# Kernel optimization log

Measured on AMD Instinct MI355X. Metric: run time of the kernel, lower is better.

Reference implementation:

```python
import jax, jax.numpy as jnp
import numpy as np

B = 65536      # batch
C = 1000       # num_classes
D = 256        # feat_dim


def _l2norm(x, eps=1e-12):
    # matches F.normalize(dim=1): v / max(||v||_2, eps)
    n = jnp.linalg.norm(x, axis=1, keepdims=True)
    return x / jnp.maximum(n, eps)


def setup_inputs() -> dict:
    key = jax.random.key(0)
    k1, k2, k3, k4, k5 = jax.random.split(key, 5)
    bound = 1.0 / np.sqrt(D)
    X = jax.random.normal(k1, (B, D), dtype=jnp.float32)
    labels = jax.random.randint(k2, (B,), 0, C)
    signatures = jax.random.uniform(k3, (C, D), dtype=jnp.float32, minval=-bound, maxval=bound)
    b_means = jax.random.uniform(k4, (1, D), dtype=jnp.float32, minval=-bound, maxval=bound)
    b_covs = jax.random.normal(k5, (D, D), dtype=jnp.float32)
    return {"X": X, "labels": labels, "signatures": signatures,
            "b_means": b_means, "b_covs": b_covs}


def reference(X, labels, signatures, b_means, b_covs):
    # SVD-based whitening of background covariance (tiny DxD)
    cov = b_covs @ b_covs.T
    U, eig, _ = jnp.linalg.svd(cov)
    DU = (eig ** -0.5)[:, None] * U.T              # diag(eig^-1/2) @ U^T, [D, D]
    xHat = _l2norm((X - b_means) @ DU.T)           # [B, D]
    sHat = _l2norm(signatures @ DU.T)              # [C, D]
    ACE_targets = xHat @ sHat.T                    # [B, C] cosine scores
    labels = labels.astype(jnp.int32)
    numerator = jnp.take_along_axis(ACE_targets, labels[:, None], axis=1)[:, 0]
    # denominator = exp(true) + sum(exp(others)) == sum over all classes
    loss = -jnp.mean(numerator - jax.nn.logsumexp(ACE_targets, axis=1))
    return (loss, ACE_targets)
```

## Files before the change

kernel.cpp:

```cpp
#include <hip/hip_runtime.h>
#include <hip/hip_bf16.h>
#include <math.h>

#define D_ 256
#define B_ 65536
#define C_ 1000

typedef _Float16 f16x8 __attribute__((ext_vector_type(8)));
typedef float f32x4 __attribute__((ext_vector_type(4)));

__global__ __launch_bounds__(256) void cov_kernel(const float* __restrict__ bc,
                                                  double* __restrict__ C64,
                                                  double* __restrict__ acc) {
  __shared__ float Ash[32][260];
  __shared__ float Bsh2[32][260];
  const int b = blockIdx.x, bi = b >> 3, bj = b & 7;
  const int e = threadIdx.x;
  if (b == 0 && e == 0) *acc = 0.0;
#pragma unroll
  for (int s = 0; s < 32; ++s) {
    int lin = s * 256 + e;
    int rr = lin >> 8, cc = lin & 255;
    Ash[rr][cc] = bc[(bi * 32 + rr) * 256 + cc];
    Bsh2[rr][cc] = bc[(bj * 32 + rr) * 256 + cc];
  }
  __syncthreads();
  const int tx = e & 15, ty = e >> 4;
  double a00 = 0, a01 = 0, a10 = 0, a11 = 0;
#pragma unroll 8
  for (int k = 0; k < 256; ++k) {
    double ar0 = (double)Ash[ty][k], ar1 = (double)Ash[ty + 16][k];
    double br0 = (double)Bsh2[tx][k], br1 = (double)Bsh2[tx + 16][k];
    a00 += ar0 * br0; a01 += ar0 * br1;
    a10 += ar1 * br0; a11 += ar1 * br1;
  }
  const int r0 = bi * 32, c0 = bj * 32;
  C64[(size_t)(r0 + ty) * D_ + c0 + tx] = a00;
  C64[(size_t)(r0 + ty) * D_ + c0 + tx + 16] = a01;
  C64[(size_t)(r0 + ty + 16) * D_ + c0 + tx] = a10;
  C64[(size_t)(r0 + ty + 16) * D_ + c0 + tx + 16] = a11;
}

__global__ __launch_bounds__(256, 1) void chol_panel(double* __restrict__ A, int p) {
  const int j0 = p * 64;
  const int r = threadIdx.x;
  __shared__ double raw[2][64];
  double pr[64];
  const bool act = (r >= j0);
  const bool inpanel = act && (r < j0 + 64);
  if (act) {
#pragma unroll
    for (int k = 0; k < 64; ++k) pr[k] = A[(size_t)r * D_ + j0 + k];
  }
  if (inpanel) raw[0][r - j0] = pr[0];
  __syncthreads();
#pragma unroll
  for (int j = 0; j < 64; ++j) {
    const int col = j0 + j;
    const double d2 = raw[j & 1][j];
    double rs = (double)rsqrtf((float)d2);
    rs = rs * (1.5 - 0.5 * d2 * rs * rs);
    rs = rs * (1.5 - 0.5 * d2 * rs * rs);
    if (r >= col) {
      const double lr_ = pr[j] * rs;
      pr[j] = lr_;
#pragma unroll
      for (int k = j + 1; k < 64; ++k) pr[k] -= lr_ * (raw[j & 1][k] * rs);
    }
    if (j < 63) {
      if (r > col && r < j0 + 64) raw[(j + 1) & 1][r - j0] = pr[j + 1];
    }
    __syncthreads();
  }
  if (act) {
    const int kmax = (r - j0 < 63) ? (r - j0) : 63;
#pragma unroll
    for (int k = 0; k < 64; ++k)
      if (k <= kmax) A[(size_t)r * D_ + j0 + k] = pr[k];
  }
}

__global__ __launch_bounds__(256) void chol_trail(double* __restrict__ A, int p) {
  const int j0 = p * 64;
  const int t0 = j0 + 64;
  int b = blockIdx.x, I = 0;
  while (b >= I + 1) { b -= I + 1; ++I; }
  const int J = b;
  const int r0 = t0 + I * 64, c0 = t0 + J * 64;
  __shared__ double LR[64][67];
  __shared__ double LC[64][67];
  const int tid = threadIdx.x;
  for (int e = tid; e < 64 * 64; e += 256) {
    int rr = e >> 6, cc = e & 63;
    LR[rr][cc] = A[(size_t)(r0 + rr) * D_ + j0 + cc];
    LC[rr][cc] = A[(size_t)(c0 + rr) * D_ + j0 + cc];
  }
  __syncthreads();
  const int tx = tid & 15, ty = tid >> 4;
  double acc[4][4];
#pragma unroll
  for (int i = 0; i < 4; ++i)
#pragma unroll
    for (int j = 0; j < 4; ++j) acc[i][j] = 0.0;
#pragma unroll 4
  for (int k = 0; k < 64; ++k) {
    double a_[4], b_[4];
#pragma unroll
    for (int i = 0; i < 4; ++i) a_[i] = LR[ty + 16 * i][k];
#pragma unroll
    for (int j = 0; j < 4; ++j) b_[j] = LC[tx + 16 * j][k];
#pragma unroll
    for (int i = 0; i < 4; ++i)
#pragma unroll
      for (int j = 0; j < 4; ++j) acc[i][j] += a_[i] * b_[j];
  }
#pragma unroll
  for (int i = 0; i < 4; ++i) {
    const int grow = r0 + ty + 16 * i;
#pragma unroll
    for (int j = 0; j < 4; ++j) {
      const int gcol = c0 + tx + 16 * j;
      A[(size_t)grow * D_ + gcol] -= acc[i][j];
    }
  }
}

__global__ __launch_bounds__(256) void inv_kernel(const double* __restrict__ L,
                                                  _Float16* __restrict__ WbP,
                                                  _Float16* __restrict__ WbT) {
  const int c = blockIdx.x;
  const int tid = threadIdx.x;
  __shared__ double w[D_];
  __shared__ double rdi[D_];
  __shared__ double rhs[32];
  __shared__ double Ldd[32][33];
  w[tid] = 0.0;
  rdi[tid] = 1.0 / L[(size_t)tid * D_ + tid];
  __syncthreads();
  const int q0 = c >> 5;
  for (int q = q0; q < 8; ++q) {
    const int i0 = q * 32;
    const int ii = tid >> 3, s = tid & 7;
    const int i = i0 + ii;
    double part = 0.0;
    for (int k = c + s; k < i0; k += 8) part += L[(size_t)i * D_ + k] * w[k];
    part += __shfl_xor(part, 1, 64);
    part += __shfl_xor(part, 2, 64);
    part += __shfl_xor(part, 4, 64);
    if (s == 0) rhs[ii] = ((i == c) ? 1.0 : 0.0) - part;
    for (int e = tid; e < 32 * 32; e += 256) {
      int rr = e >> 5, cc = e & 31;
      Ldd[rr][cc] = L[(size_t)(i0 + rr) * D_ + i0 + cc];
    }
    __syncthreads();
    if (tid < 32) {
      double x = rhs[tid];
      double v = 0.0;
      for (int j = 0; j < 32; ++j) {
        double xj = __shfl(x, j, 64);
        double wj = xj * rdi[i0 + j];
        if (tid == j) v = wj;
        if (tid > j) x -= Ldd[tid][j] * wj;
      }
      w[i0 + tid] = v;
    }
    __syncthreads();
  }
  _Float16 h = (_Float16)(float)w[tid];
  WbT[(size_t)c * D_ + tid] = h;
  {
    const int g = tid >> 4, lrr = tid & 15;
    const int ks = c >> 5, lqq = (c >> 3) & 3, jj = c & 7;
    WbP[(size_t)(g * 8 + ks) * 512 + (size_t)(lqq * 16 + lrr) * 8 + jj] = h;
  }
}

__global__ void sig_kernel(const float* __restrict__ S, const _Float16* __restrict__ WbT,
                           _Float16* __restrict__ sHatP) {
  int c = blockIdx.x, i = threadIdx.x;
  const int g = c >> 4, lr = c & 15;
  const int ks = i >> 5, lq = (i >> 3) & 3, jj = i & 7;
  const size_t off = (size_t)(g * 8 + ks) * 512 + (size_t)(lq * 16 + lr) * 8 + jj;
  if (c >= C_) { sHatP[off] = (_Float16)0.0f; return; }
  __shared__ float srow[D_];
  __shared__ float wred[4];
  srow[i] = S[c * D_ + i];
  __syncthreads();
  float t = 0.f;
  for (int k = 0; k < D_; ++k) t += (float)WbT[k * D_ + i] * srow[k];
  float ss = t * t;
#pragma unroll
  for (int d = 1; d < 64; d <<= 1) ss += __shfl_xor(ss, d, 64);
  if ((i & 63) == 0) wred[i >> 6] = ss;
  __syncthreads();
  float tot = wred[0] + wred[1] + wred[2] + wred[3];
  float rn = 1.0f / fmaxf(sqrtf(tot), 1e-12f);
  sHatP[off] = (_Float16)(t * rn);
}

__global__ __launch_bounds__(512) void xform_kernel(const float* __restrict__ X,
                                                    const float* __restrict__ means,
                                                    const _Float16* __restrict__ WbP,
                                                    _Float16* __restrict__ xHat,
                                                    float* __restrict__ rnX) {
  __shared__ __align__(16) _Float16 Wsh[65536];
  __shared__ float msh[D_];
  const int tid = threadIdx.x;
  const int wid = tid >> 6, l = tid & 63, lr = l & 15, lq = l >> 4;
  const int rowbase = blockIdx.x * 128;
  const int arow = rowbase + wid * 16 + lr;
  if (tid < 256) msh[tid] = means[tid];
#pragma unroll
  for (int s = 0; s < 16; ++s) {
    const int off = (wid * 16 + s) * 512;
    __builtin_amdgcn_global_load_lds(
        (const __attribute__((address_space(1))) unsigned int*)(WbP + off + l * 8),
        (__attribute__((address_space(3))) unsigned int*)(&Wsh[off]), 16, 0, 0);
  }
  __syncthreads();

  f16x8 af[8];
#pragma unroll
  for (int ks = 0; ks < 8; ++ks) {
    const float* xp = X + (size_t)arow * D_ + lq * 8 + ks * 32;
    const float4 x0 = *(const float4*)(xp);
    const float4 x1 = *(const float4*)(xp + 4);
    const int mb = lq * 8 + ks * 32;
    af[ks][0] = (_Float16)(x0.x - msh[mb + 0]);
    af[ks][1] = (_Float16)(x0.y - msh[mb + 1]);
    af[ks][2] = (_Float16)(x0.z - msh[mb + 2]);
    af[ks][3] = (_Float16)(x0.w - msh[mb + 3]);
    af[ks][4] = (_Float16)(x1.x - msh[mb + 4]);
    af[ks][5] = (_Float16)(x1.y - msh[mb + 5]);
    af[ks][6] = (_Float16)(x1.z - msh[mb + 6]);
    af[ks][7] = (_Float16)(x1.w - msh[mb + 7]);
  }

  float ss[4] = {0.f, 0.f, 0.f, 0.f};
  const _Float16* bb = &Wsh[(size_t)l * 8];
  for (int ch = 0; ch < 2; ++ch) {
    f32x4 acc[8];
#pragma unroll
    for (int t = 0; t < 8; ++t) acc[t] = (f32x4){0.f, 0.f, 0.f, 0.f};
#pragma unroll
    for (int ks = 0; ks < 8; ++ks) {
#pragma unroll
      for (int t = 0; t < 8; ++t) {
        f16x8 bf = *(const f16x8*)(bb + (ch * 64 + t * 8 + ks) * 512);
        acc[t] = __builtin_amdgcn_mfma_f32_16x16x32_f16(af[ks], bf, acc[t], 0, 0, 0);
      }
    }
#pragma unroll
    for (int t = 0; t < 8; ++t) {
      const int col = ch * 128 + t * 16 + lr;
#pragma unroll
      for (int j = 0; j < 4; ++j) {
        const int row = rowbase + wid * 16 + lq * 4 + j;
        float v = acc[t][j];
        ss[j] += v * v;
        xHat[(size_t)row * D_ + col] = (_Float16)v;
      }
    }
  }
#pragma unroll
  for (int d = 1; d < 16; d <<= 1) {
#pragma unroll
    for (int j = 0; j < 4; ++j) ss[j] += __shfl_xor(ss[j], d, 64);
  }
  if (lr == 0) {
#pragma unroll
    for (int j = 0; j < 4; ++j) {
      const int row = rowbase + wid * 16 + lq * 4 + j;
      rnX[row] = 1.0f / fmaxf(sqrtf(ss[j]), 1e-12f);
    }
  }
}

__global__ __launch_bounds__(1024) void ace_kernel(const _Float16* __restrict__ xHat,
                                                   const _Float16* __restrict__ sHatP,
                                                   const float* __restrict__ rnX,
                                                   const int* __restrict__ labels,
                                                   float* __restrict__ outACE,
                                                   double* __restrict__ acc_loss) {
  __shared__ __align__(16) _Float16 Bsh[2][64 * 512];
  __shared__ float part[64];
  const int tid = threadIdx.x;
  const int wid = tid >> 6, l = tid & 63, lr = l & 15, lq = l >> 4;
  const int rowbase = blockIdx.x * 256;
  const int wrow = rowbase + wid * 16;

  f16x8 a[8];
  {
    const _Float16* ap = xHat + (size_t)(wrow + lr) * D_ + lq * 8;
#pragma unroll
    for (int ks = 0; ks < 8; ++ks) a[ks] = *(const f16x8*)(ap + ks * 32);
  }

  int lab[4]; float rx[4], ssum[4], num[4];
#pragma unroll
  for (int j = 0; j < 4; ++j) {
    int row = wrow + lq * 4 + j;
    lab[j] = labels[row];
    rx[j] = rnX[row];
    ssum[j] = 0.f; num[j] = 0.f;
  }

#define STAGE(bufi, chi) do {                                                        \
    const _Float16* _src = sHatP + (size_t)(chi) * 32768;                            \
    _Float16* _dst = &Bsh[bufi][0];                                                  \
    _Pragma("unroll")                                                                \
    for (int _s = 0; _s < 4; ++_s) {                                                 \
      const int _off = wid * 2048 + _s * 512;                                        \
      __builtin_amdgcn_global_load_lds(                                              \
          (const __attribute__((address_space(1))) unsigned int*)(_src + _off + l * 8), \
          (__attribute__((address_space(3))) unsigned int*)(_dst + _off), 16, 0, 0); \
    } } while (0)

  float* const outrow = outACE + (size_t)(wrow + lq * 4) * C_;

  STAGE(0, 0);
  __syncthreads();
  int buf = 0;
  for (int ch = 0; ch < 8; ++ch) {
    if (ch < 7) {
      STAGE(buf ^ 1, ch + 1);
      __builtin_amdgcn_sched_barrier(0);
    }
    const _Float16* bb = &Bsh[buf][(size_t)l * 8];
    f32x4 acc[8];
#pragma unroll
    for (int t = 0; t < 8; ++t) acc[t] = (f32x4){0.f, 0.f, 0.f, 0.f};
#pragma unroll
    for (int ks = 0; ks < 8; ++ks) {
#pragma unroll
      for (int t = 0; t < 8; ++t) {
        f16x8 bf = *(const f16x8*)(bb + (t * 8 + ks) * 512);
        acc[t] = __builtin_amdgcn_mfma_f32_16x16x32_f16(a[ks], bf, acc[t], 0, 0, 0);
      }
    }
#pragma unroll
    for (int t = 0; t < 8; ++t) {
      const int col = ch * 128 + t * 16 + lr;
      const bool valid = (col < C_);
#pragma unroll
      for (int j = 0; j < 4; ++j) {
        float v = acc[t][j] * rx[j];
        if (valid) outrow[(size_t)j * C_ + col] = v;
        ssum[j] += __expf(v - 1.0f);
        num[j] = (col == lab[j]) ? v : num[j];
      }
    }
    if (ch < 7) {
      __builtin_amdgcn_sched_barrier(0);
      asm volatile("s_waitcnt vmcnt(32)" ::: "memory");
      __builtin_amdgcn_s_barrier();
      __builtin_amdgcn_sched_barrier(0);
    }
    buf ^= 1;
  }
#undef STAGE

#pragma unroll
  for (int d2 = 1; d2 < 16; d2 <<= 1) {
#pragma unroll
    for (int j = 0; j < 4; ++j) {
      ssum[j] += __shfl_xor(ssum[j], d2, 64);
      num[j]  += __shfl_xor(num[j], d2, 64);
    }
  }
  if (lr == 0) {
    const float padcorr = 24.0f * __expf(-1.0f);
    float contrib = 0.f;
#pragma unroll
    for (int j = 0; j < 4; ++j)
      contrib += num[j] - (1.0f + __logf(ssum[j] - padcorr));
    part[wid * 4 + lq] = contrib;
  }
  __syncthreads();
  if (tid == 0) {
    float s = 0.f;
#pragma unroll
    for (int p2 = 0; p2 < 64; ++p2) s += part[p2];
    atomicAdd(acc_loss, (double)s);
  }
}

__global__ void fin_kernel(const double* a, float* out) {
  out[0] = (float)(-(*a) / (double)B_);
}

extern "C" void kernel_launch(void* const* d_in, const int* in_sizes, int n_in,
                              void* d_out, int out_size, void* d_ws, size_t ws_size,
                              hipStream_t stream) {
  const float* X      = (const float*)d_in[0];
  const int*   labels = (const int*)d_in[1];
  const float* S      = (const float*)d_in[2];
  const float* means  = (const float*)d_in[3];
  const float* bc     = (const float*)d_in[4];
  float* out = (float*)d_out;

  char* w = (char*)d_ws;
  double*    acc   = (double*)(w + 0);
  double*    C64   = (double*)(w + 256);
  _Float16*  WbP   = (_Float16*)(w + 524544);
  _Float16*  WbT   = (_Float16*)(w + 655616);
  _Float16*  sHatP = (_Float16*)(w + 786688);
  float*     rnX   = (float*)(w + 1310976);
  _Float16*  xHat  = (_Float16*)(w + 1573120);

  cov_kernel<<<64, 256, 0, stream>>>(bc, C64, acc);
  for (int p = 0; p < 4; ++p) {
    chol_panel<<<1, 256, 0, stream>>>(C64, p);
    int nt = 3 - p;
    if (nt > 0) chol_trail<<<nt * (nt + 1) / 2, 256, 0, stream>>>(C64, p);
  }
  inv_kernel<<<256, 256, 0, stream>>>(C64, WbP, WbT);
  sig_kernel<<<1024, 256, 0, stream>>>(S, WbT, sHatP);
  xform_kernel<<<512, 512, 0, stream>>>(X, means, WbP, xHat, rnX);
  ace_kernel<<<256, 1024, 0, stream>>>(xHat, sHatP, rnX, labels, out + 1, acc);
  fin_kernel<<<1, 1, 0, stream>>>(acc, out);
}
```

Before: 367.5 us.

## Fuse whitening transform into ACE kernel and finalize loss via last-block counter

Merges the X whitening/normalization GEMM into the ACE score kernel. The whitened rows are computed in registers, passed through swizzled LDS into the A-fragment layout, and never written to global memory as xHat/rnX. The separate finalize launch is replaced by an atomic counter, so the last block writes the mean loss. This removes a 32MB fp16 round trip and two kernel launches. In exchange each block holds 16 accumulator tiles, which raises register pressure, and the whole 128KB LDS is reused across phases with extra barriers.

Result: faster. 358.5 us (-2.5%).

```diff
diff --git a/kernel.cpp b/kernel.cpp
--- a/kernel.cpp
+++ b/kernel.cpp
@@ -11,12 +11,13 @@
 
 __global__ __launch_bounds__(256) void cov_kernel(const float* __restrict__ bc,
                                                   double* __restrict__ C64,
-                                                  double* __restrict__ acc) {
+                                                  double* __restrict__ acc,
+                                                  unsigned int* __restrict__ counter) {
   __shared__ float Ash[32][260];
   __shared__ float Bsh2[32][260];
   const int b = blockIdx.x, bi = b >> 3, bj = b & 7;
   const int e = threadIdx.x;
-  if (b == 0 && e == 0) *acc = 0.0;
+  if (b == 0 && e == 0) { *acc = 0.0; *counter = 0u; }
 #pragma unroll
   for (int s = 0; s < 32; ++s) {
     int lin = s * 256 + e;
@@ -198,24 +199,35 @@
   sHatP[off] = (_Float16)(t * rn);
 }
 
-__global__ __launch_bounds__(512) void xform_kernel(const float* __restrict__ X,
-                                                    const float* __restrict__ means,
-                                                    const _Float16* __restrict__ WbP,
-                                                    _Float16* __restrict__ xHat,
-                                                    float* __restrict__ rnX) {
-  __shared__ __align__(16) _Float16 Wsh[65536];
+__global__ __launch_bounds__(1024) void ace_kernel(const float* __restrict__ X,
+                                                   const float* __restrict__ means,
+                                                   const _Float16* __restrict__ WbP,
+                                                   const _Float16* __restrict__ sHatP,
+                                                   const int* __restrict__ labels,
+                                                   float* __restrict__ out,
+                                                   double* __restrict__ acc_loss,
+                                                   unsigned int* __restrict__ counter) {
+  __shared__ __align__(16) char ldsraw[131072];
   __shared__ float msh[D_];
+  __shared__ float part[64];
+  _Float16* const Wsh = (_Float16*)ldsraw;
+  char* const xsC = ldsraw;
+  _Float16* const Bsh = (_Float16*)ldsraw;
+  float* const outACE = out + 1;
+
   const int tid = threadIdx.x;
   const int wid = tid >> 6, l = tid & 63, lr = l & 15, lq = l >> 4;
-  const int rowbase = blockIdx.x * 128;
-  const int arow = rowbase + wid * 16 + lr;
+  const int rowbase = blockIdx.x * 256;
+  const int wrow = rowbase + wid * 16;
+  const int arow = wrow + lr;
+
   if (tid < 256) msh[tid] = means[tid];
 #pragma unroll
-  for (int s = 0; s < 16; ++s) {
-    const int off = (wid * 16 + s) * 512;
+  for (int s = 0; s < 8; ++s) {
+    const int off = (wid * 8 + s) * 512;
     __builtin_amdgcn_global_load_lds(
         (const __attribute__((address_space(1))) unsigned int*)(WbP + off + l * 8),
-        (__attribute__((address_space(3))) unsigned int*)(&Wsh[off]), 16, 0, 0);
+        (__attribute__((address_space(3))) unsigned int*)(Wsh + off), 16, 0, 0);
   }
   __syncthreads();
 
@@ -235,79 +247,67 @@
     af[ks][6] = (_Float16)(x1.z - msh[mb + 6]);
     af[ks][7] = (_Float16)(x1.w - msh[mb + 7]);
   }
-
+  f32x4 wacc[16];
+#pragma unroll
+  for (int u = 0; u < 16; ++u) wacc[u] = (f32x4){0.f, 0.f, 0.f, 0.f};
+  {
+    const _Float16* wb = Wsh + (size_t)l * 8;
+#pragma unroll
+    for (int ks = 0; ks < 8; ++ks) {
+#pragma unroll
+      for (int u = 0; u < 16; ++u) {
+        f16x8 bf = *(const f16x8*)(wb + (u * 8 + ks) * 512);
+        wacc[u] = __builtin_amdgcn_mfma_f32_16x16x32_f16(af[ks], bf, wacc[u], 0, 0, 0);
+      }
+    }
+  }
   float ss[4] = {0.f, 0.f, 0.f, 0.f};
-  const _Float16* bb = &Wsh[(size_t)l * 8];
-  for (int ch = 0; ch < 2; ++ch) {
-    f32x4 acc[8];
-#pragma unroll
-    for (int t = 0; t < 8; ++t) acc[t] = (f32x4){0.f, 0.f, 0.f, 0.f};
-#pragma unroll
-    for (int ks = 0; ks < 8; ++ks) {
-#pragma unroll
-      for (int t = 0; t < 8; ++t) {
-        f16x8 bf = *(const f16x8*)(bb + (ch * 64 + t * 8 + ks) * 512);
-        acc[t] = __builtin_amdgcn_mfma_f32_16x16x32_f16(af[ks], bf, acc[t], 0, 0, 0);
-      }
-    }
-#pragma unroll
-    for (int t = 0; t < 8; ++t) {
-      const int col = ch * 128 + t * 16 + lr;
-#pragma unroll
-      for (int j = 0; j < 4; ++j) {
-        const int row = rowbase + wid * 16 + lq * 4 + j;
-        float v = acc[t][j];
-        ss[j] += v * v;
-        xHat[(size_t)row * D_ + col] = (_Float16)v;
-      }
-    }
-  }
+#pragma unroll
+  for (int u = 0; u < 16; ++u)
+#pragma unroll
+    for (int j = 0; j < 4; ++j) ss[j] += wacc[u][j] * wacc[u][j];
 #pragma unroll
   for (int d = 1; d < 16; d <<= 1) {
 #pragma unroll
     for (int j = 0; j < 4; ++j) ss[j] += __shfl_xor(ss[j], d, 64);
   }
-  if (lr == 0) {
+  float rx[4];
+#pragma unroll
+  for (int j = 0; j < 4; ++j) rx[j] = 1.0f / fmaxf(sqrtf(ss[j]), 1e-12f);
+
+  __syncthreads();
+
+#pragma unroll
+  for (int u = 0; u < 16; ++u) {
 #pragma unroll
     for (int j = 0; j < 4; ++j) {
-      const int row = rowbase + wid * 16 + lq * 4 + j;
-      rnX[row] = 1.0f / fmaxf(sqrtf(ss[j]), 1e-12f);
-    }
-  }
-}
-
-__global__ __launch_bounds__(1024) void ace_kernel(const _Float16* __restrict__ xHat,
-                                                   const _Float16* __restrict__ sHatP,
-                                                   const float* __restrict__ rnX,
-                                                   const int* __restrict__ labels,
-                                                   float* __restrict__ outACE,
-                                                   double* __restrict__ acc_loss) {
-  __shared__ __align__(16) _Float16 Bsh[2][64 * 512];
-  __shared__ float part[64];
-  const int tid = threadIdx.x;
-  const int wid = tid >> 6, l = tid & 63, lr = l & 15, lq = l >> 4;
-  const int rowbase = blockIdx.x * 256;
-  const int wrow = rowbase + wid * 16;
-
+      const int rowl = wid * 16 + lq * 4 + j;
+      const int byte = (rowl * 512 + (u * 16 + lr) * 2) ^ ((rowl & 7) << 4);
+      *(_Float16*)(xsC + byte) = (_Float16)wacc[u][j];
+    }
+  }
+  __syncthreads();
   f16x8 a[8];
   {
-    const _Float16* ap = xHat + (size_t)(wrow + lr) * D_ + lq * 8;
-#pragma unroll
-    for (int ks = 0; ks < 8; ++ks) a[ks] = *(const f16x8*)(ap + ks * 32);
-  }
-
-  int lab[4]; float rx[4], ssum[4], num[4];
+    const int rowA = wid * 16 + lr;
+#pragma unroll
+    for (int ks = 0; ks < 8; ++ks) {
+      const int byte = (rowA * 512 + ks * 64 + lq * 16) ^ ((rowA & 7) << 4);
+      a[ks] = *(const f16x8*)(xsC + byte);
+    }
+  }
+  __syncthreads();
+
+  int lab[4]; float ssum[4], num[4];
 #pragma unroll
   for (int j = 0; j < 4; ++j) {
-    int row = wrow + lq * 4 + j;
-    lab[j] = labels[row];
-    rx[j] = rnX[row];
+    lab[j] = labels[wrow + lq * 4 + j];
     ssum[j] = 0.f; num[j] = 0.f;
   }
 
 #define STAGE(bufi, chi) do {                                                        \
     const _Float16* _src = sHatP + (size_t)(chi) * 32768;                            \
-    _Float16* _dst = &Bsh[bufi][0];                                                  \
+    _Float16* _dst = Bsh + (size_t)(bufi) * 32768;                                   \
     _Pragma("unroll")                                                                \
     for (int _s = 0; _s < 4; ++_s) {                                                 \
       const int _off = wid * 2048 + _s * 512;                                        \
@@ -326,7 +326,7 @@
       STAGE(buf ^ 1, ch + 1);
       __builtin_amdgcn_sched_barrier(0);
     }
-    const _Float16* bb = &Bsh[buf][(size_t)l * 8];
+    const _Float16* bb = Bsh + (size_t)buf * 32768 + (size_t)l * 8;
     f32x4 acc[8];
 #pragma unroll
     for (int t = 0; t < 8; ++t) acc[t] = (f32x4){0.f, 0.f, 0.f, 0.f};
@@ -382,11 +382,14 @@
 #pragma unroll
     for (int p2 = 0; p2 < 64; ++p2) s += part[p2];
     atomicAdd(acc_loss, (double)s);
-  }
-}
-
-__global__ void fin_kernel(const double* a, float* out) {
-  out[0] = (float)(-(*a) / (double)B_);
+    __threadfence();
+    unsigned int old = atomicAdd(counter, 1u);
+    if (old == (unsigned int)(gridDim.x - 1)) {
+      __threadfence();
+      double tot = atomicAdd(acc_loss, 0.0);
+      out[0] = (float)(-tot / (double)B_);
+    }
+  }
 }
 
 extern "C" void kernel_launch(void* const* d_in, const int* in_sizes, int n_in,
@@ -400,15 +403,14 @@
   float* out = (float*)d_out;
 
   char* w = (char*)d_ws;
-  double*    acc   = (double*)(w + 0);
-  double*    C64   = (double*)(w + 256);
-  _Float16*  WbP   = (_Float16*)(w + 524544);
-  _Float16*  WbT   = (_Float16*)(w + 655616);
-  _Float16*  sHatP = (_Float16*)(w + 786688);
-  float*     rnX   = (float*)(w + 1310976);
-  _Float16*  xHat  = (_Float16*)(w + 1573120);
-
-  cov_kernel<<<64, 256, 0, stream>>>(bc, C64, acc);
+  double*       acc   = (double*)(w + 0);
+  unsigned int* cnt   = (unsigned int*)(w + 128);
+  double*       C64   = (double*)(w + 256);
+  _Float16*     WbP   = (_Float16*)(w + 524544);
+  _Float16*     WbT   = (_Float16*)(w + 655616);
+  _Float16*     sHatP = (_Float16*)(w + 786688);
+
+  cov_kernel<<<64, 256, 0, stream>>>(bc, C64, acc, cnt);
   for (int p = 0; p < 4; ++p) {
     chol_panel<<<1, 256, 0, stream>>>(C64, p);
     int nt = 3 - p;
@@ -416,7 +418,5 @@
   }
   inv_kernel<<<256, 256, 0, stream>>>(C64, WbP, WbT);
   sig_kernel<<<1024, 256, 0, stream>>>(S, WbT, sHatP);
-  xform_kernel<<<512, 512, 0, stream>>>(X, means, WbP, xHat, rnX);
-  ace_kernel<<<256, 1024, 0, stream>>>(xHat, sHatP, rnX, labels, out + 1, acc);
-  fin_kernel<<<1, 1, 0, stream>>>(acc, out);
-}
+  ace_kernel<<<256, 1024, 0, stream>>>(X, means, WbP, sHatP, labels, out, acc, cnt);
+}
```
